# Performance work log

Measured on AMD Instinct MI355X. Metric: run time of the kernel, lower is better.

## Reference

```python
import jax, jax.numpy as jnp
import numpy as np

# ---- config (matches init_kwargs) ----
C_IN, C_OUT = 128, 128
HYPER_OUT = 64            # hyper_out_size in DoubleConv
KB = C_IN // HYPER_OUT    # k = 2 blocks along input channels
HB = C_OUT // HYPER_OUT   # h = 2 blocks along output channels
Z_DIM, HID, SEIDEL_DIM = 128, 128, 48
R, F = 8, 3               # num_radii, filter size
BN_EPS = 1e-5


def _mlp_bank(z, W1, b1, W2, b2):
    # z: (S,); W1: (M,S,HID); returns (M, HID) embeddings from M distinct MLPs
    h = jax.nn.relu(jnp.einsum('s,msh->mh', z, W1) + b1)
    return jax.nn.relu(jnp.einsum('mh,mhg->mg', h, W2) + b2)


def _hyper(e, hw2, hb2, hw1, hb1):
    # Ha-style hypernetwork: e (Z_DIM,) -> kernel (64, 64, R, F, F)
    h_in = (e @ hw2 + hb2).reshape(HYPER_OUT, Z_DIM)
    h_fin = h_in @ hw1 + hb1  # (64, 64*R*F*F)
    return h_fin.reshape(HYPER_OUT, HYPER_OUT, R, F, F)


def _assemble(kernels, rows, cols):
    # kernels: (rows*cols, 64, 64, R, F, F) -> (rows*64, cols*64, R, F, F)
    k = kernels.reshape(rows, cols, HYPER_OUT, HYPER_OUT, R, F, F)
    k = k.transpose(0, 2, 1, 3, 4, 5, 6)
    return k.reshape(rows * HYPER_OUT, cols * HYPER_OUT, R, F, F)


def _interp_radii(w, Wdim):
    # trilinear interpolate (R,F,F)->(Wdim,F,F); F->F is identity, so linear along R
    # align_corners=False (PyTorch default)
    src = (jnp.arange(Wdim, dtype=jnp.float32) + 0.5) * (R / Wdim) - 0.5
    src = jnp.clip(src, 0.0, R - 1.0)
    i0 = jnp.floor(src).astype(jnp.int32)
    i1 = jnp.minimum(i0 + 1, R - 1)
    t = (src - i0.astype(jnp.float32))[None, None, :, None, None]
    return w[:, :, i0] * (1.0 - t) + w[:, :, i1] * t  # (co, ci, Wdim, F, F)


def _lri_conv(x, w):
    # x: (c_in, H, W); w: (c_out, c_in, R, F, F); padding=1, k=3
    c_in, H, W = x.shape
    xp = jnp.concatenate([x[:, -1:, :], x, x[:, :1, :]], axis=1)  # circular pad H
    xp = jnp.pad(xp, ((0, 0), (0, 0), (1, 1)))                    # zero pad W
    # patches laid out (c, di, dj) to match F.unfold
    pat = jnp.stack([xp[:, di:di + H, dj:dj + W]
                     for di in range(3) for dj in range(3)], axis=1)  # (c_in, 9, H, W)
    pat = pat.reshape(c_in * 9, H, W).transpose(1, 2, 0)              # (H, W, c_in*9)
    wi = _interp_radii(w, W)                                          # (co, ci, W, F, F)
    wu = wi.transpose(0, 2, 1, 3, 4).reshape(w.shape[0], W, c_in * 9) # (co, W, ci*9)
    return jnp.einsum('hwj,cwj->chw', pat, wu)                        # (co, H, W)


def _bn_eval(x, gamma, beta):
    # eval-mode BatchNorm2d with running_mean=0, running_var=1
    scale = gamma / jnp.sqrt(1.0 + BN_EPS)
    return x * scale[:, None, None] + beta[:, None, None]


def setup_inputs() -> dict:
    key = jax.random.key(0)
    ks = jax.random.split(key, 20)
    B, H, W = 2, 256, 128
    n1 = HB * KB   # 4 MLPs for first conv
    n2 = HB * HB   # 4 MLPs for second conv
    inp = {
        'x': jax.random.normal(ks[0], (B, C_IN, H, W), jnp.float32),
        'seidel': jax.random.normal(ks[1], (B, SEIDEL_DIM), jnp.float32),
        'm1_W1': jax.random.normal(ks[2], (n1, SEIDEL_DIM, HID)) * 0.1,
        'm1_b1': jnp.zeros((n1, HID)),
        'm1_W2': jax.random.normal(ks[3], (n1, HID, HID)) * 0.08,
        'm1_b2': jnp.zeros((n1, HID)),
        'm2_W1': jax.random.normal(ks[4], (n2, SEIDEL_DIM, HID)) * 0.1,
        'm2_b1': jnp.zeros((n2, HID)),
        'm2_W2': jax.random.normal(ks[5], (n2, HID, HID)) * 0.08,
        'm2_b2': jnp.zeros((n2, HID)),
        'hyp_w2': jax.random.normal(ks[6], (Z_DIM, HYPER_OUT * Z_DIM)) * 0.02,
        'hyp_b2': jnp.zeros((HYPER_OUT * Z_DIM,)),
        'hyp_w1': jax.random.normal(ks[7], (Z_DIM, HYPER_OUT * R * F * F)) * 0.02,
        'hyp_b1': jnp.zeros((HYPER_OUT * R * F * F,)),
        'bn1_g': jnp.ones((C_OUT,)), 'bn1_b': jnp.zeros((C_OUT,)),
        'bn2_g': jnp.ones((C_OUT,)), 'bn2_b': jnp.zeros((C_OUT,)),
    }
    return inp


def reference(x, seidel, m1_W1, m1_b1, m1_W2, m1_b2, m2_W1, m2_b1, m2_W2, m2_b2,
              hyp_w2, hyp_b2, hyp_w1, hyp_b1, bn1_g, bn1_b, bn2_g, bn2_b):
    hyper = lambda e: _hyper(e, hyp_w2, hyp_b2, hyp_w1, hyp_b1)

    def one_sample(x_i, z_i):
        emb1 = _mlp_bank(z_i, m1_W1, m1_b1, m1_W2, m1_b2)   # (h*k, Z)
        w1 = _assemble(jax.vmap(hyper)(emb1), HB, KB)        # (c_out, c_in, R, F, F)
        emb2 = _mlp_bank(z_i, m2_W1, m2_b1, m2_W2, m2_b2)   # (h*h, Z)
        w2 = _assemble(jax.vmap(hyper)(emb2), HB, HB)        # (c_out, c_out, R, F, F)
        y = jax.nn.relu(_bn_eval(_lri_conv(x_i, w1), bn1_g, bn1_b))
        y = jax.nn.relu(_bn_eval(_lri_conv(y, w2), bn2_g, bn2_b))
        return y

    return jax.vmap(one_sample)(x, seidel)  # (B, c_out, H, W)
```

## Files before the change

kernel.cpp:

```cpp
#include <hip/hip_runtime.h>
#include <hip/hip_bf16.h>

typedef _Float16 f16;
typedef _Float16 half8 __attribute__((ext_vector_type(8)));
typedef _Float16 half4_t __attribute__((ext_vector_type(4)));
typedef float floatx16 __attribute__((ext_vector_type(16)));

__device__ __forceinline__ void gll16(const void* g, void* l) {
    __builtin_amdgcn_global_load_lds(
        (const __attribute__((address_space(1))) void*)g,
        (__attribute__((address_space(3))) void*)l, 16, 0, 0);
}

__global__ __launch_bounds__(256) void embed_a(
    const float* __restrict__ seidel,
    const float* __restrict__ m1W1, const float* __restrict__ m1b1,
    const float* __restrict__ m1W2, const float* __restrict__ m1b2,
    const float* __restrict__ m2W1, const float* __restrict__ m2b1,
    const float* __restrict__ m2W2, const float* __restrict__ m2b2,
    float* __restrict__ eout)
{
    int combo = blockIdx.x;
    int s = combo >> 3, conv = (combo >> 2) & 1, m = combo & 3;
    const float* W1 = conv ? m2W1 : m1W1;
    const float* b1 = conv ? m2b1 : m1b1;
    const float* W2 = conv ? m2W2 : m1W2;
    const float* b2 = conv ? m2b2 : m1b2;
    __shared__ float zs[48], hbuf[128];
    int tid = threadIdx.x;
    if (tid < 48) zs[tid] = seidel[s*48 + tid];
    __syncthreads();
    if (tid < 128) {
        float a = b1[m*128 + tid];
        for (int i = 0; i < 48; ++i) a += zs[i] * W1[(m*48 + i)*128 + tid];
        hbuf[tid] = fmaxf(a, 0.f);
    }
    __syncthreads();
    if (tid < 128) {
        float a = b2[m*128 + tid];
        for (int i = 0; i < 128; ++i) a += hbuf[i] * W2[(m*128 + i)*128 + tid];
        eout[combo*128 + tid] = fmaxf(a, 0.f);
    }
}

__global__ __launch_bounds__(128) void embed_b3(
    const float* __restrict__ eout, const float* __restrict__ hw2,
    const float* __restrict__ hb2, float* __restrict__ hin)
{
    __shared__ float es[16][128];
    int tid = threadIdx.x;
    int j = blockIdx.x*128 + tid;
    for (int i = tid; i < 2048; i += 128) es[i >> 7][i & 127] = eout[i];
    __syncthreads();
    float acc[16];
    float b = hb2[j];
    #pragma unroll
    for (int c = 0; c < 16; ++c) acc[c] = b;
    for (int i = 0; i < 128; ++i) {
        float wv = hw2[(size_t)i*8192 + j];
        #pragma unroll
        for (int c = 0; c < 16; ++c) acc[c] += es[c][i]*wv;
    }
    #pragma unroll
    for (int c = 0; c < 16; ++c) hin[(size_t)c*8192 + j] = acc[c];
}

__global__ void hw1t_kernel(const float* __restrict__ in, float* __restrict__ out)
{
    __shared__ float tile[32][33];
    int j0 = blockIdx.x*32, k0 = blockIdx.y*32;
    int tx = threadIdx.x, ty = threadIdx.y;
    #pragma unroll
    for (int i = 0; i < 4; ++i) tile[ty + i*8][tx] = in[(size_t)(k0 + ty + i*8)*4608 + j0 + tx];
    __syncthreads();
    #pragma unroll
    for (int i = 0; i < 4; ++i) out[(size_t)(j0 + ty + i*8)*128 + k0 + tx] = tile[tx][ty + i*8];
}

__global__ __launch_bounds__(256) void hfin3_kernel(
    const float* __restrict__ hin, const float* __restrict__ hw1t,
    const float* __restrict__ hb1, f16* __restrict__ wtab)
{
    int c72 = blockIdx.x;
    int combo = blockIdx.y;
    int r = c72 / 9, tap = c72 - r*9;
    int s = combo >> 3, conv = (combo >> 2) & 1, m = combo & 3;
    __shared__ f16 A[64][136];
    __shared__ f16 B[64][136];
    __shared__ f16 ct[64][72];
    int tid = threadIdx.x;
    const float4* hsrc = (const float4*)(hin + (size_t)combo*8192);
    for (int i = tid; i < 2048; i += 256) {
        int a = i >> 5, k4 = (i & 31)*4;
        float4 v = hsrc[i];
        half4_t h; h[0]=(f16)v.x; h[1]=(f16)v.y; h[2]=(f16)v.z; h[3]=(f16)v.w;
        *(half4_t*)&A[a][k4] = h;
    }
    for (int i = tid; i < 2048; i += 256) {
        int b = i >> 5, k4 = (i & 31)*4;
        float4 v = *(const float4*)(hw1t + (size_t)(b*72 + c72)*128 + k4);
        half4_t h; h[0]=(f16)v.x; h[1]=(f16)v.y; h[2]=(f16)v.z; h[3]=(f16)v.w;
        *(half4_t*)&B[b][k4] = h;
    }
    __syncthreads();
    int lane = tid & 63, wid = tid >> 6;
    int wa = wid & 1, wb = wid >> 1;
    int l31 = lane & 31, lq = lane >> 5;
    floatx16 c = (floatx16)0.f;
    #pragma unroll
    for (int k = 0; k < 8; ++k) {
        half8 af = *(const half8*)&A[wa*32 + l31][k*16 + lq*8];
        half8 bf = *(const half8*)&B[wb*32 + l31][k*16 + lq*8];
        c = __builtin_amdgcn_mfma_f32_32x32x16_f16(af, bf, c, 0, 0, 0);
    }
    int bcol = wb*32 + l31;
    float bias = hb1[bcol*72 + c72];
    #pragma unroll
    for (int rr = 0; rr < 16; ++rr) {
        int a = wa*32 + (rr & 3) + 8*(rr >> 2) + 4*lq;
        ct[a][bcol] = (f16)(c[rr] + bias);
    }
    __syncthreads();
    {
        int a = tid & 63, q = tid >> 6;
        int hc = (m & 1)*4 + q;
        int co = (m >> 1)*64 + a;
        f16* dst = wtab + (((((size_t)(s*2 + conv)*8 + r)*8 + hc)*9 + tap)*128 + co)*16;
        *(half8*)(dst)     = *(const half8*)&ct[a][q*16];
        *(half8*)(dst + 8) = *(const half8*)&ct[a][q*16 + 8];
    }
}

__global__ __launch_bounds__(256) void xpose_cast2(
    const float* __restrict__ in, f16* __restrict__ out, float4* __restrict__ zerop)
{
    __shared__ f16 tileT[128*136];
    int h = blockIdx.x, s = blockIdx.y;
    int tid = threadIdx.x;
    if (h == 0 && s == 0 && tid < 4) zerop[tid] = make_float4(0.f, 0.f, 0.f, 0.f);
    int cg = tid >> 5, q2 = tid & 31;
    const float* src = in + (size_t)s*4194304 + (size_t)h*128;
    for (int pass = 0; pass < 16; ++pass) {
        int c = pass*8 + cg;
        float4 v = *(const float4*)(src + (size_t)c*32768 + q2*4);
        tileT[(q2*4 + 0)*136 + c] = (f16)v.x;
        tileT[(q2*4 + 1)*136 + c] = (f16)v.y;
        tileT[(q2*4 + 2)*136 + c] = (f16)v.z;
        tileT[(q2*4 + 3)*136 + c] = (f16)v.w;
    }
    __syncthreads();
    int ww = tid >> 1, hf = tid & 1;
    const f16* srcT = &tileT[ww*136 + hf*64];
    f16* dst = out + (((size_t)(s*128 + ww)*256 + h)*128) + hf*64;
    #pragma unroll
    for (int i = 0; i < 8; ++i)
        *(float4*)(dst + i*8) = *(const float4*)(srcT + i*8);
}

__global__ void xpose_out(const float* __restrict__ in, float* __restrict__ out)
{
    __shared__ float tile[32][33];
    int sc = blockIdx.z;
    int w0 = blockIdx.x*32, h0 = blockIdx.y*32;
    int tx = threadIdx.x, ty = threadIdx.y;
    const float* src = in + ((size_t)sc*128 + w0)*256 + h0;
    #pragma unroll
    for (int i = 0; i < 4; ++i) tile[ty + i*8][tx] = src[(size_t)(ty + i*8)*256 + tx];
    __syncthreads();
    float* dst = out + ((size_t)sc*256 + h0)*128 + w0;
    #pragma unroll
    for (int i = 0; i < 4; ++i) dst[(size_t)(ty + i*8)*128 + tx] = tile[tx][ty + i*8];
}

template<int OUT_F16>
__global__ __launch_bounds__(512) void conv_mfma10(
    const f16* __restrict__ xin,
    const f16* __restrict__ wtab,
    int conv,
    const float* __restrict__ bng, const float* __restrict__ bnb,
    void* __restrict__ outp,
    const float4* __restrict__ zerop)
{
    int b = blockIdx.x;
    int xcd = b & 7, i = b >> 3;
    int s = xcd >> 2;
    int w = (xcd & 3)*32 + i;
    const f16* xs  = xin  + (size_t)s*4194304;
    const f16* wts = wtab + (size_t)(s*2 + conv)*1179648;

    float fsrc = fminf(fmaxf((w + 0.5f)*0.0625f - 0.5f, 0.f), 7.f);
    int r0 = (int)fsrc, r1 = min(r0 + 1, 7);
    float tf = fsrc - (float)r0;
    f16 th = (f16)tf;
    bool interp = (tf != 0.f);

    __shared__ __align__(16) char sbuf[49152];

    int tid = threadIdx.x;
    int lane = tid & 63, wid = tid >> 6;
    int wc = wid & 1, wh = wid >> 1;
    int l31 = lane & 31, lq = lane >> 5;

    floatx16 acc[2][2];
    #pragma unroll
    for (int a = 0; a < 2; ++a)
        #pragma unroll
        for (int c = 0; c < 2; ++c) acc[a][c] = (floatx16)0.f;

    auto stage = [&](int bsel, int hc) {
        char* xb = sbuf + bsel*24576;
        #pragma unroll
        for (int it = 0; it < 3; ++it) {
            int id = it*512 + tid;
            int dj = id >> 9, part = (id >> 8) & 1, hp = id & 255;
            int wsg = w + dj - 1;
            const void* src = (wsg >= 0 && wsg < 128)
                ? (const void*)(xs + ((size_t)wsg*256 + hp)*128 + hc*16 + part*8)
                : (const void*)zerop;
            gll16(src, xb + (size_t)(it*512 + wid*64)*16);
        }
    };

    stage(0, 0);
    __syncthreads();

    int aoff = (wc*64 + l31)*16 + lq*8;
    for (int hc = 0; hc < 8; ++hc) {
        int cur = hc & 1;
        if (hc < 7) stage(cur ^ 1, hc + 1);
        const f16* xb = (const f16*)(sbuf + cur*24576);
        const f16* p0 = wts + (size_t)(r0*8 + hc)*18432 + aoff;
        const f16* p1 = wts + (size_t)(r1*8 + hc)*18432 + aoff;
        __builtin_amdgcn_s_setprio(1);
        #pragma unroll
        for (int tap = 0; tap < 9; ++tap) {
            int di = tap/3, dj = tap - di*3;
            half8 a0 = *(const half8*)(p0 + tap*2048);
            half8 a1 = *(const half8*)(p0 + tap*2048 + 512);
            if (interp) {
                half8 q0 = *(const half8*)(p1 + tap*2048);
                half8 q1 = *(const half8*)(p1 + tap*2048 + 512);
                a0 = a0 + (q0 - a0)*th;
                a1 = a1 + (q1 - a1)*th;
            }
            int h0 = wh*64 + l31 + di - 1;
            half8 bf0 = *(const half8*)(xb + (size_t)(dj*512 + lq*256 + (h0 & 255))*8);
            half8 bf1 = *(const half8*)(xb + (size_t)(dj*512 + lq*256 + ((h0 + 32) & 255))*8);
            acc[0][0] = __builtin_amdgcn_mfma_f32_32x32x16_f16(a0, bf0, acc[0][0], 0, 0, 0);
            acc[0][1] = __builtin_amdgcn_mfma_f32_32x32x16_f16(a0, bf1, acc[0][1], 0, 0, 0);
            acc[1][0] = __builtin_amdgcn_mfma_f32_32x32x16_f16(a1, bf0, acc[1][0], 0, 0, 0);
            acc[1][1] = __builtin_amdgcn_mfma_f32_32x32x16_f16(a1, bf1, acc[1][1], 0, 0, 0);
        }
        __builtin_amdgcn_s_setprio(0);
        __syncthreads();
    }

    float rs = rsqrtf(1.f + 1e-5f);
    if (OUT_F16) {
        f16* otile = (f16*)sbuf;
        f16* yout = (f16*)outp + ((size_t)(s*128 + w)*256)*128;
        #pragma unroll
        for (int ph = 0; ph < 2; ++ph) {
            __syncthreads();
            if ((wh >> 1) == ph) {
                #pragma unroll
                for (int ct = 0; ct < 2; ++ct) {
                    #pragma unroll
                    for (int ht = 0; ht < 2; ++ht) {
                        int hrow = (wh & 1)*64 + ht*32 + l31;
                        #pragma unroll
                        for (int rq = 0; rq < 4; ++rq) {
                            int cb = wc*64 + ct*32 + rq*8 + lq*4;
                            float4 g4 = *(const float4*)&bng[cb];
                            float4 b4 = *(const float4*)&bnb[cb];
                            half4_t v;
                            #pragma unroll
                            for (int e = 0; e < 4; ++e) {
                                float g = (&g4.x)[e], bb = (&b4.x)[e];
                                v[e] = (f16)fmaxf(acc[ct][ht][rq*4 + e]*g*rs + bb, 0.f);
                            }
                            *(half4_t*)&otile[hrow*136 + cb] = v;
                        }
                    }
                }
            }
            __syncthreads();
            {
                int hrow = tid >> 2, qc = tid & 3;
                const f16* srcT = &otile[hrow*136 + qc*32];
                f16* d = yout + (size_t)(ph*128 + hrow)*128 + qc*32;
                #pragma unroll
                for (int k = 0; k < 4; ++k)
                    *(float4*)(d + k*8) = *(const float4*)(srcT + k*8);
            }
        }
    } else {
        #pragma unroll
        for (int ct = 0; ct < 2; ++ct) {
            #pragma unroll
            for (int ht = 0; ht < 2; ++ht) {
                int hrow = wh*64 + ht*32 + l31;
                #pragma unroll
                for (int r = 0; r < 16; ++r) {
                    int co = wc*64 + ct*32 + (r & 3) + 8*(r >> 2) + 4*lq;
                    float v = fmaxf(acc[ct][ht][r]*bng[co]*rs + bnb[co], 0.f);
                    ((float*)outp)[((size_t)(s*128 + co)*128 + w)*256 + hrow] = v;
                }
            }
        }
    }
}

extern "C" void kernel_launch(void* const* d_in, const int* in_sizes, int n_in,
                              void* d_out, int out_size, void* d_ws, size_t ws_size,
                              hipStream_t stream) {
    const float* x      = (const float*)d_in[0];
    const float* seidel = (const float*)d_in[1];
    const float* m1W1 = (const float*)d_in[2];
    const float* m1b1 = (const float*)d_in[3];
    const float* m1W2 = (const float*)d_in[4];
    const float* m1b2 = (const float*)d_in[5];
    const float* m2W1 = (const float*)d_in[6];
    const float* m2b1 = (const float*)d_in[7];
    const float* m2W2 = (const float*)d_in[8];
    const float* m2b2 = (const float*)d_in[9];
    const float* hw2  = (const float*)d_in[10];
    const float* hb2  = (const float*)d_in[11];
    const float* hw1  = (const float*)d_in[12];
    const float* hb1  = (const float*)d_in[13];
    const float* bn1g = (const float*)d_in[14];
    const float* bn1b = (const float*)d_in[15];
    const float* bn2g = (const float*)d_in[16];
    const float* bn2b = (const float*)d_in[17];
    float* outp = (float*)d_out;

    char* wsb = (char*)d_ws;
    f16*   wtab = (f16*)wsb;
    f16*   y1t  = (f16*)(wsb + 9437184);
    f16*   xt   = (f16*)(wsb + 26214400);
    float* y2t  = (float*)(wsb + 26214400);
    float4* zerop = (float4*)(wsb + 59768832);
    float* hin  = (float*)(wsb + 26214400);
    float* eout = (float*)(wsb + 26214400 + 524288);
    float* hw1t = (float*)(wsb + 26214400 + 1048576);

    embed_a<<<16, 256, 0, stream>>>(seidel, m1W1, m1b1, m1W2, m1b2,
                                    m2W1, m2b1, m2W2, m2b2, eout);
    embed_b3<<<64, 128, 0, stream>>>(eout, hw2, hb2, hin);
    hw1t_kernel<<<dim3(144, 4), dim3(32, 8), 0, stream>>>(hw1, hw1t);
    hfin3_kernel<<<dim3(72, 16), 256, 0, stream>>>(hin, hw1t, hb1, wtab);
    xpose_cast2<<<dim3(256, 2), 256, 0, stream>>>(x, xt, zerop);
    conv_mfma10<1><<<256, 512, 0, stream>>>(xt, wtab, 0, bn1g, bn1b, (void*)y1t, zerop);
    conv_mfma10<0><<<256, 512, 0, stream>>>(y1t, wtab, 1, bn2g, bn2b, (void*)y2t, zerop);
    xpose_out<<<dim3(4, 8, 256), dim3(32, 8), 0, stream>>>(y2t, outp);
}
```

Measured before the change: 162.9 us.

## Stage interpolated conv weights through double-buffered LDS with register prefetch

```diff
diff --git a/kernel.cpp b/kernel.cpp
--- a/kernel.cpp
+++ b/kernel.cpp
@@ -123,9 +123,10 @@
     __syncthreads();
     {
         int a = tid & 63, q = tid >> 6;
-        int hc = (m & 1)*4 + q;
+        int chunk = (m & 1)*2 + (q >> 1);
         int co = (m >> 1)*64 + a;
-        f16* dst = wtab + (((((size_t)(s*2 + conv)*8 + r)*8 + hc)*9 + tap)*128 + co)*16;
+        f16* dst = wtab + (((((size_t)(s*2 + conv)*8 + r)*4 + chunk)*9 + tap)*128 + co)*32
+                   + (q & 1)*16;
         *(half8*)(dst)     = *(const half8*)&ct[a][q*16];
         *(half8*)(dst + 8) = *(const half8*)&ct[a][q*16 + 8];
     }
@@ -173,7 +174,7 @@
 }
 
 template<int OUT_F16>
-__global__ __launch_bounds__(512) void conv_mfma10(
+__global__ __launch_bounds__(512, 1) void conv_mfma11(
     const f16* __restrict__ xin,
     const f16* __restrict__ wtab,
     int conv,
@@ -190,11 +191,9 @@
 
     float fsrc = fminf(fmaxf((w + 0.5f)*0.0625f - 0.5f, 0.f), 7.f);
     int r0 = (int)fsrc, r1 = min(r0 + 1, 7);
-    float tf = fsrc - (float)r0;
-    f16 th = (f16)tf;
-    bool interp = (tf != 0.f);
-
-    __shared__ __align__(16) char sbuf[49152];
+    f16 th = (f16)(fsrc - (float)r0);
+
+    __shared__ __align__(16) char sbuf[122880];
 
     int tid = threadIdx.x;
     int lane = tid & 63, wid = tid >> 6;
@@ -207,8 +206,25 @@
         #pragma unroll
         for (int c = 0; c < 2; ++c) acc[a][c] = (floatx16)0.f;
 
-    auto stage = [&](int bsel, int hc) {
-        char* xb = sbuf + bsel*24576;
+    half8 wa[5], wb[5];
+
+    auto loadw = [&](int hc) {
+        int chunk = hc >> 1, half = hc & 1;
+        #pragma unroll
+        for (int p = 0; p < 5; ++p) {
+            int sl = p*512 + tid;
+            if (sl < 2304) {
+                int tap = sl >> 8, rem = sl & 255;
+                int part = rem >> 7, co = rem & 127;
+                size_t off = (size_t)co*32 + half*16 + part*8;
+                wa[p] = *(const half8*)(wts + (((size_t)(r0*4 + chunk)*9 + tap) << 12) + off);
+                wb[p] = *(const half8*)(wts + (((size_t)(r1*4 + chunk)*9 + tap) << 12) + off);
+            }
+            asm volatile("" : "+v"(wa[p]), "+v"(wb[p]));
+        }
+    };
+    auto stage_x = [&](int bsel, int hc) {
+        char* xb = sbuf + 73728 + bsel*24576;
         #pragma unroll
         for (int it = 0; it < 3; ++it) {
             int id = it*512 + tid;
@@ -220,36 +236,59 @@
             gll16(src, xb + (size_t)(it*512 + wid*64)*16);
         }
     };
-
-    stage(0, 0);
-    __syncthreads();
-
-    int aoff = (wc*64 + l31)*16 + lq*8;
+    auto write_w = [&](int bsel) {
+        char* wbase = sbuf + bsel*36864;
+        #pragma unroll
+        for (int p = 0; p < 5; ++p) {
+            int sl = p*512 + tid;
+            if (sl < 2304) {
+                half8 o = wa[p] + (wb[p] - wa[p])*th;
+                *(half8*)(wbase + (size_t)sl*16) = o;
+            }
+        }
+    };
+
+    loadw(0);
+    stage_x(0, 0);
+    write_w(0);
+    __syncthreads();
+
+    #pragma unroll 2
     for (int hc = 0; hc < 8; ++hc) {
         int cur = hc & 1;
-        if (hc < 7) stage(cur ^ 1, hc + 1);
-        const f16* xb = (const f16*)(sbuf + cur*24576);
-        const f16* p0 = wts + (size_t)(r0*8 + hc)*18432 + aoff;
-        const f16* p1 = wts + (size_t)(r1*8 + hc)*18432 + aoff;
+        if (hc < 7) { loadw(hc + 1); stage_x(cur ^ 1, hc + 1); }
+        const char* wbuf = sbuf + cur*36864;
+        const f16* xb = (const f16*)(sbuf + 73728 + cur*24576);
+
         __builtin_amdgcn_s_setprio(1);
         #pragma unroll
-        for (int tap = 0; tap < 9; ++tap) {
+        for (int tap = 0; tap < 4; ++tap) {
             int di = tap/3, dj = tap - di*3;
-            half8 a0 = *(const half8*)(p0 + tap*2048);
-            half8 a1 = *(const half8*)(p0 + tap*2048 + 512);
-            if (interp) {
-                half8 q0 = *(const half8*)(p1 + tap*2048);
-                half8 q1 = *(const half8*)(p1 + tap*2048 + 512);
-                a0 = a0 + (q0 - a0)*th;
-                a1 = a1 + (q1 - a1)*th;
-            }
+            half8 af0 = *(const half8*)(wbuf + (size_t)(tap*256 + lq*128 + wc*64 + l31)*16);
+            half8 af1 = *(const half8*)(wbuf + (size_t)(tap*256 + lq*128 + wc*64 + 32 + l31)*16);
             int h0 = wh*64 + l31 + di - 1;
             half8 bf0 = *(const half8*)(xb + (size_t)(dj*512 + lq*256 + (h0 & 255))*8);
             half8 bf1 = *(const half8*)(xb + (size_t)(dj*512 + lq*256 + ((h0 + 32) & 255))*8);
-            acc[0][0] = __builtin_amdgcn_mfma_f32_32x32x16_f16(a0, bf0, acc[0][0], 0, 0, 0);
-            acc[0][1] = __builtin_amdgcn_mfma_f32_32x32x16_f16(a0, bf1, acc[0][1], 0, 0, 0);
-            acc[1][0] = __builtin_amdgcn_mfma_f32_32x32x16_f16(a1, bf0, acc[1][0], 0, 0, 0);
-            acc[1][1] = __builtin_amdgcn_mfma_f32_32x32x16_f16(a1, bf1, acc[1][1], 0, 0, 0);
+            acc[0][0] = __builtin_amdgcn_mfma_f32_32x32x16_f16(af0, bf0, acc[0][0], 0, 0, 0);
+            acc[0][1] = __builtin_amdgcn_mfma_f32_32x32x16_f16(af0, bf1, acc[0][1], 0, 0, 0);
+            acc[1][0] = __builtin_amdgcn_mfma_f32_32x32x16_f16(af1, bf0, acc[1][0], 0, 0, 0);
+            acc[1][1] = __builtin_amdgcn_mfma_f32_32x32x16_f16(af1, bf1, acc[1][1], 0, 0, 0);
+        }
+        __builtin_amdgcn_s_setprio(0);
+        if (hc < 7) write_w(cur ^ 1);
+        __builtin_amdgcn_s_setprio(1);
+        #pragma unroll
+        for (int tap = 4; tap < 9; ++tap) {
+            int di = tap/3, dj = tap - di*3;
+            half8 af0 = *(const half8*)(wbuf + (size_t)(tap*256 + lq*128 + wc*64 + l31)*16);
+            half8 af1 = *(const half8*)(wbuf + (size_t)(tap*256 + lq*128 + wc*64 + 32 + l31)*16);
+            int h0 = wh*64 + l31 + di - 1;
+            half8 bf0 = *(const half8*)(xb + (size_t)(dj*512 + lq*256 + (h0 & 255))*8);
+            half8 bf1 = *(const half8*)(xb + (size_t)(dj*512 + lq*256 + ((h0 + 32) & 255))*8);
+            acc[0][0] = __builtin_amdgcn_mfma_f32_32x32x16_f16(af0, bf0, acc[0][0], 0, 0, 0);
+            acc[0][1] = __builtin_amdgcn_mfma_f32_32x32x16_f16(af0, bf1, acc[0][1], 0, 0, 0);
+            acc[1][0] = __builtin_amdgcn_mfma_f32_32x32x16_f16(af1, bf0, acc[1][0], 0, 0, 0);
+            acc[1][1] = __builtin_amdgcn_mfma_f32_32x32x16_f16(af1, bf1, acc[1][1], 0, 0, 0);
         }
         __builtin_amdgcn_s_setprio(0);
         __syncthreads();
@@ -350,7 +389,7 @@
     hw1t_kernel<<<dim3(144, 4), dim3(32, 8), 0, stream>>>(hw1, hw1t);
     hfin3_kernel<<<dim3(72, 16), 256, 0, stream>>>(hin, hw1t, hb1, wtab);
     xpose_cast2<<<dim3(256, 2), 256, 0, stream>>>(x, xt, zerop);
-    conv_mfma10<1><<<256, 512, 0, stream>>>(xt, wtab, 0, bn1g, bn1b, (void*)y1t, zerop);
-    conv_mfma10<0><<<256, 512, 0, stream>>>(y1t, wtab, 1, bn2g, bn2b, (void*)y2t, zerop);
+    conv_mfma11<1><<<256, 512, 0, stream>>>(xt, wtab, 0, bn1g, bn1b, (void*)y1t, zerop);
+    conv_mfma11<0><<<256, 512, 0, stream>>>(y1t, wtab, 1, bn2g, bn2b, (void*)y2t, zerop);
     xpose_out<<<dim3(4, 8, 256), dim3(32, 8), 0, stream>>>(y2t, outp);
 }
```

Result: faster. 141.0 us (-13.4%).
